# Performance work log

Measured on AMD Instinct MI355X. Metric: run time of the kernel, lower is better.

Reference implementation:

```python
import jax, jax.numpy as jnp
import numpy as np

L = 10           # outer iterations (module arg L -> sinkhorn n_iter)
N_INNER = 1      # n_inner_iter=1 in SinkhornLoss.forward
EPS = 1.0        # entropic regularization epsilon


def setup_inputs() -> dict:
    key = jax.random.key(0)
    kx, ky = jax.random.split(key)
    x = jax.random.normal(kx, (8192, 32), dtype=jnp.float32)
    y = jax.random.normal(ky, (8192, 32), dtype=jnp.float32)
    return {"x": x, "y": y}


def _sinkhorn_loss(x, y):
    n, m = x.shape[0], y.shape[0]
    # sqeuclidean cdist: [n, m]
    C = (x * x).sum(1)[:, None] + (y * y).sum(1)[None, :] - 2.0 * (x @ y.T)
    # uniform marginals mu = 1/n, nu = 1/m (mu=None, nu=None in source)
    logmu = -jnp.log(jnp.asarray(n, C.dtype))
    lognu = -jnp.log(jnp.asarray(m, C.dtype))
    f0 = jnp.zeros((n,), C.dtype)
    g0 = jnp.zeros((m,), C.dtype)

    def body(carry, _):
        f, g = carry
        # log-domain Sinkhorn updates (stable logsumexp form)
        f = EPS * (logmu - jax.nn.logsumexp((g[None, :] - C) / EPS, axis=1))
        g = EPS * (lognu - jax.nn.logsumexp((f[:, None] - C) / EPS, axis=0))
        return (f, g), None

    (f, g), _ = jax.lax.scan(body, (f0, g0), None, length=L * N_INNER)
    gamma = jnp.exp((f[:, None] + g[None, :] - C) / EPS)  # transport plan [n, m]
    return jnp.sum(C * gamma)  # min_cost = <C, gamma>


def reference(x, y):
    return _sinkhorn_loss(x, y)
```

## Files before the change

kernel.cpp:

```cpp
#include <hip/hip_runtime.h>
#include <math.h>


#define KDIM 32
#define NPS 32
#define NSL_LOSS 16
#define LOG2E 1.44269504088896340736f

typedef short short8 __attribute__((ext_vector_type(8)));
typedef float f32x4 __attribute__((ext_vector_type(4)));

__device__ __forceinline__ unsigned short f2bf(float f) {
    unsigned int u = __float_as_uint(f);
    u += 0x7FFF + ((u >> 16) & 1);
    return (unsigned short)(u >> 16);
}
__device__ __forceinline__ float bf2f(unsigned short b) {
    return __uint_as_float(((unsigned int)b) << 16);
}

__global__ void prep_split(const float* __restrict__ x, const float* __restrict__ y,
                           int nelem,
                           unsigned short* __restrict__ xh, unsigned short* __restrict__ xl,
                           unsigned short* __restrict__ yh, unsigned short* __restrict__ yl) {
    int i4 = (blockIdx.x * 256 + threadIdx.x) * 4;
    if (i4 >= 2 * nelem) return;
    const float* src; unsigned short* dh; unsigned short* dl; int off;
    if (i4 < nelem) { src = x; dh = xh; dl = xl; off = i4; }
    else            { src = y; dh = yh; dl = yl; off = i4 - nelem; }
    float4 v = *(const float4*)(src + off);
    ushort4 h, l;
    h.x = f2bf(v.x); l.x = f2bf(v.x - bf2f(h.x));
    h.y = f2bf(v.y); l.y = f2bf(v.y - bf2f(h.y));
    h.z = f2bf(v.z); l.z = f2bf(v.z - bf2f(h.z));
    h.w = f2bf(v.w); l.w = f2bf(v.w - bf2f(h.w));
    *(ushort4*)(dh + off) = h;
    *(ushort4*)(dl + off) = l;
}

__global__ void prep_sq(const float* __restrict__ x, const float* __restrict__ y,
                        int n, float* __restrict__ xsq, float* __restrict__ ysq,
                        float* __restrict__ b_l2e) {
    int i = blockIdx.x * blockDim.x + threadIdx.x;
    if (i >= 2 * n) return;
    const float* src = (i < n) ? x : y;
    int r = (i < n) ? i : i - n;
    const float4* p = (const float4*)(src + (size_t)r * KDIM);
    float s = 0.f;
#pragma unroll
    for (int q = 0; q < 8; ++q) {
        float4 v = p[q];
        s += v.x * v.x + v.y * v.y + v.z * v.z + v.w * v.w;
    }
    if (i < n) xsq[r] = s;
    else { ysq[r] = s; b_l2e[r] = -LOG2E * s; }
}

__global__ __launch_bounds__(256, 4) void sink_pass(
    const unsigned short* __restrict__ Ah, const unsigned short* __restrict__ Alo,
    const unsigned short* __restrict__ Bh, const unsigned short* __restrict__ Blo,
    const float* __restrict__ bias_direct,
    const float* __restrict__ psum_in,
    float* __restrict__ psum_out, int n, float base_l2e) {
    __shared__ float biasl[256];
    __shared__ float red[4][64][17];

    const int tid = threadIdx.x;
    const int w = tid >> 6, lane = tid & 63;
    const int mrow = lane & 15, quad = lane >> 4, koff = quad * 8;
    const int i0 = (blockIdx.x * 4 + w) * 64;
    const int jbeg = blockIdx.y * (n / NPS);

    {
        int c = jbeg + tid;
        float b;
        if (bias_direct) {
            b = bias_direct[c];
        } else {
            float s = 0.f;
#pragma unroll
            for (int k = 0; k < NPS; ++k) s += psum_in[(size_t)k * n + c];
            b = base_l2e - __log2f(s);
        }
        biasl[tid] = b;
    }

    short8 aH[4], aL[4];
#pragma unroll
    for (int t = 0; t < 4; ++t) {
        size_t rb = (size_t)(i0 + t * 16 + mrow) * KDIM + koff;
        aH[t] = *(const short8*)(Ah + rb);
        aL[t] = *(const short8*)(Alo + rb);
    }
    __syncthreads();

    float rs[16];
#pragma unroll
    for (int q = 0; q < 16; ++q) rs[q] = 0.f;
    const float c2 = 2.0f * LOG2E;

    for (int jt = 0; jt < n / NPS; jt += 32) {
        const int j0 = jbeg + jt;
        short8 bH[2], bL[2]; float bc[2];
#pragma unroll
        for (int u = 0; u < 2; ++u) {
            size_t rb = (size_t)(j0 + u * 16 + mrow) * KDIM + koff;
            bH[u] = *(const short8*)(Bh + rb);
            bL[u] = *(const short8*)(Blo + rb);
            bc[u] = biasl[jt + u * 16 + mrow];
        }
#pragma unroll
        for (int t = 0; t < 4; ++t)
#pragma unroll
            for (int u = 0; u < 2; ++u) {
                f32x4 z = {0.f, 0.f, 0.f, 0.f};
                z = __builtin_amdgcn_mfma_f32_16x16x32_bf16(aH[t], bH[u], z, 0, 0, 0);
                z = __builtin_amdgcn_mfma_f32_16x16x32_bf16(aH[t], bL[u], z, 0, 0, 0);
                z = __builtin_amdgcn_mfma_f32_16x16x32_bf16(aL[t], bH[u], z, 0, 0, 0);
#pragma unroll
                for (int r = 0; r < 4; ++r)
                    rs[t * 4 + r] += __builtin_amdgcn_exp2f(fmaf(z[r], c2, bc[u]));
            }
    }

#pragma unroll
    for (int t = 0; t < 4; ++t)
#pragma unroll
        for (int r = 0; r < 4; ++r)
            red[w][t * 16 + quad * 4 + r][mrow] = rs[t * 4 + r];
    __syncthreads();
    {
        int w2 = tid >> 6, row = tid & 63;
        float s = 0.f;
#pragma unroll
        for (int c = 0; c < 16; ++c) s += red[w2][row][c];
        psum_out[(size_t)blockIdx.y * n + (blockIdx.x * 4 + w2) * 64 + row] = s;
    }
}

__global__ __launch_bounds__(256, 4) void sink_loss(
    const unsigned short* __restrict__ Xh, const unsigned short* __restrict__ Xl,
    const unsigned short* __restrict__ Yh, const unsigned short* __restrict__ Yl,
    const float* __restrict__ apsum, const float* __restrict__ bpsum,
    const float* __restrict__ xsq, const float* __restrict__ ysq,
    float* __restrict__ partials, int n, float base_l2e) {
    __shared__ float bcl[512];
    __shared__ float ysl[512];
    __shared__ float arowl[128];
    __shared__ float xsl[128];
    __shared__ float red[256];

    const int tid = threadIdx.x;
    const int w = tid >> 6, lane = tid & 63;
    const int mrow = lane & 15, quad = lane >> 4, koff = quad * 8;
    const int i0 = (blockIdx.x * 4 + w) * 32;
    const int jbeg = blockIdx.y * (n / NSL_LOSS);

#pragma unroll
    for (int h = 0; h < 2; ++h) {
        int c = tid + h * 256;
        int j = jbeg + c;
        float s = 0.f;
#pragma unroll
        for (int k = 0; k < NPS; ++k) s += bpsum[(size_t)k * n + j];
        bcl[c] = base_l2e - __log2f(s);
        ysl[c] = ysq[j];
    }
    if (tid < 128) {
        int i = blockIdx.x * 128 + tid;
        float s = 0.f;
#pragma unroll
        for (int k = 0; k < NPS; ++k) s += apsum[(size_t)k * n + i];
        arowl[tid] = base_l2e - __log2f(s);
        xsl[tid] = xsq[i];
    }

    short8 aH[2], aL[2];
#pragma unroll
    for (int t = 0; t < 2; ++t) {
        size_t rb = (size_t)(i0 + t * 16 + mrow) * KDIM + koff;
        aH[t] = *(const short8*)(Xh + rb);
        aL[t] = *(const short8*)(Xl + rb);
    }
    __syncthreads();

    float ar[8], xs[8];
#pragma unroll
    for (int t = 0; t < 2; ++t)
#pragma unroll
        for (int r = 0; r < 4; ++r) {
            int rl = w * 32 + t * 16 + quad * 4 + r;
            ar[t * 4 + r] = arowl[rl];
            xs[t * 4 + r] = xsl[rl];
        }

    const float c2 = 2.0f * LOG2E;
    float acc = 0.f;

    for (int jt = 0; jt < n / NSL_LOSS; jt += 32) {
        short8 bH[2], bL[2]; float bc[2], ysv[2];
#pragma unroll
        for (int u = 0; u < 2; ++u) {
            int cl = jt + u * 16 + mrow;
            size_t rb = (size_t)(jbeg + cl) * KDIM + koff;
            bH[u] = *(const short8*)(Yh + rb);
            bL[u] = *(const short8*)(Yl + rb);
            bc[u] = bcl[cl];
            ysv[u] = ysl[cl];
        }
#pragma unroll
        for (int t = 0; t < 2; ++t)
#pragma unroll
            for (int u = 0; u < 2; ++u) {
                f32x4 z = {0.f, 0.f, 0.f, 0.f};
                z = __builtin_amdgcn_mfma_f32_16x16x32_bf16(aH[t], bH[u], z, 0, 0, 0);
                z = __builtin_amdgcn_mfma_f32_16x16x32_bf16(aH[t], bL[u], z, 0, 0, 0);
                z = __builtin_amdgcn_mfma_f32_16x16x32_bf16(aL[t], bH[u], z, 0, 0, 0);
#pragma unroll
                for (int r = 0; r < 4; ++r) {
                    float dd = z[r];
                    float wgt = __builtin_amdgcn_exp2f(fmaf(dd, c2, ar[t * 4 + r] + bc[u]));
                    float cst = fmaf(dd, -2.f, xs[t * 4 + r] + ysv[u]);
                    acc = fmaf(cst, wgt, acc);
                }
            }
    }

    red[tid] = acc;
    __syncthreads();
#pragma unroll
    for (int s = 128; s > 0; s >>= 1) {
        if (tid < s) red[tid] += red[tid + s];
        __syncthreads();
    }
    if (tid == 0) partials[blockIdx.y * gridDim.x + blockIdx.x] = red[0];
}

__global__ void sink_reduce(const float* __restrict__ p, int nb,
                            float* __restrict__ out) {
    __shared__ float red[256];
    int tid = threadIdx.x;
    float v = 0.f;
    for (int i = tid; i < nb; i += 256) v += p[i];
    red[tid] = v;
    __syncthreads();
#pragma unroll
    for (int s = 128; s > 0; s >>= 1) {
        if (tid < s) red[tid] += red[tid + s];
        __syncthreads();
    }
    if (tid == 0) out[0] = red[0];
}

extern "C" void kernel_launch(void* const* d_in, const int* in_sizes, int n_in,
                              void* d_out, int out_size, void* d_ws, size_t ws_size,
                              hipStream_t stream) {
    const float* x = (const float*)d_in[0];
    const float* y = (const float*)d_in[1];
    const int n = in_sizes[0] / KDIM;
    const int nelem = n * KDIM;
    const float base_l2e = -LOG2E * logf((float)n);

    float* ws = (float*)d_ws;
    float* xsq   = ws;
    float* ysq   = ws + n;
    float* b_l2e = ws + 2 * n;
    float* apsum = ws + 3 * n;
    float* bpsum = ws + (3 + NPS) * n;
    float* part  = ws + (3 + 2 * NPS) * n;
    unsigned short* us = (unsigned short*)(ws + (4 + 2 * NPS) * n);
    unsigned short* xh = us;
    unsigned short* xl = us + nelem;
    unsigned short* yh = us + 2 * nelem;
    unsigned short* yl = us + 3 * nelem;

    dim3 pgrid(n / 256, NPS);
    dim3 lgrid(n / 128, NSL_LOSS);

    prep_split<<<(2 * nelem / 4 + 255) / 256, 256, 0, stream>>>(x, y, nelem, xh, xl, yh, yl);
    prep_sq<<<(2 * n + 255) / 256, 256, 0, stream>>>(x, y, n, xsq, ysq, b_l2e);

    sink_pass<<<pgrid, 256, 0, stream>>>(xh, xl, yh, yl, b_l2e, nullptr, apsum, n, base_l2e);
    sink_pass<<<pgrid, 256, 0, stream>>>(yh, yl, xh, xl, nullptr, apsum, bpsum, n, base_l2e);
    for (int t = 1; t < 10; ++t) {
        sink_pass<<<pgrid, 256, 0, stream>>>(xh, xl, yh, yl, nullptr, bpsum, apsum, n, base_l2e);
        sink_pass<<<pgrid, 256, 0, stream>>>(yh, yl, xh, xl, nullptr, apsum, bpsum, n, base_l2e);
    }
    sink_loss<<<lgrid, 256, 0, stream>>>(xh, xl, yh, yl, apsum, bpsum, xsq, ysq, part, n, base_l2e);
    sink_reduce<<<1, 256, 0, stream>>>(part, (n / 128) * NSL_LOSS, (float*)d_out);
}
```

Before: 447.9 us.

## Prescale x by 2·log2e, use multiplicative exp-domain potentials, and double-buffer B loads

```diff
diff --git a/kernel.cpp b/kernel.cpp
--- a/kernel.cpp
+++ b/kernel.cpp
@@ -6,6 +6,7 @@
 #define NPS 32
 #define NSL_LOSS 16
 #define LOG2E 1.44269504088896340736f
+#define LN2 0.69314718055994530942f
 
 typedef short short8 __attribute__((ext_vector_type(8)));
 typedef float f32x4 __attribute__((ext_vector_type(4)));
@@ -25,10 +26,11 @@
                            unsigned short* __restrict__ yh, unsigned short* __restrict__ yl) {
     int i4 = (blockIdx.x * 256 + threadIdx.x) * 4;
     if (i4 >= 2 * nelem) return;
-    const float* src; unsigned short* dh; unsigned short* dl; int off;
-    if (i4 < nelem) { src = x; dh = xh; dl = xl; off = i4; }
-    else            { src = y; dh = yh; dl = yl; off = i4 - nelem; }
+    const float* src; unsigned short* dh; unsigned short* dl; int off; float sc;
+    if (i4 < nelem) { src = x; dh = xh; dl = xl; off = i4; sc = 2.0f * LOG2E; }
+    else            { src = y; dh = yh; dl = yl; off = i4 - nelem; sc = 1.0f; }
     float4 v = *(const float4*)(src + off);
+    v.x *= sc; v.y *= sc; v.z *= sc; v.w *= sc;
     ushort4 h, l;
     h.x = f2bf(v.x); l.x = f2bf(v.x - bf2f(h.x));
     h.y = f2bf(v.y); l.y = f2bf(v.y - bf2f(h.y));
@@ -40,7 +42,7 @@
 
 __global__ void prep_sq(const float* __restrict__ x, const float* __restrict__ y,
                         int n, float* __restrict__ xsq, float* __restrict__ ysq,
-                        float* __restrict__ b_l2e) {
+                        float* __restrict__ pb0) {
     int i = blockIdx.x * blockDim.x + threadIdx.x;
     if (i >= 2 * n) return;
     const float* src = (i < n) ? x : y;
@@ -53,16 +55,16 @@
         s += v.x * v.x + v.y * v.y + v.z * v.z + v.w * v.w;
     }
     if (i < n) xsq[r] = s;
-    else { ysq[r] = s; b_l2e[r] = -LOG2E * s; }
+    else { ysq[r] = s; pb0[r] = __builtin_amdgcn_exp2f(-LOG2E * s); }
 }
 
 __global__ __launch_bounds__(256, 4) void sink_pass(
     const unsigned short* __restrict__ Ah, const unsigned short* __restrict__ Alo,
     const unsigned short* __restrict__ Bh, const unsigned short* __restrict__ Blo,
-    const float* __restrict__ bias_direct,
+    const float* __restrict__ pb_direct,
     const float* __restrict__ psum_in,
-    float* __restrict__ psum_out, int n, float base_l2e) {
-    __shared__ float biasl[256];
+    float* __restrict__ psum_out, int n, float inv_n) {
+    __shared__ float pbl[256];
     __shared__ float red[4][64][17];
 
     const int tid = threadIdx.x;
@@ -74,15 +76,15 @@
     {
         int c = jbeg + tid;
         float b;
-        if (bias_direct) {
-            b = bias_direct[c];
+        if (pb_direct) {
+            b = pb_direct[c];
         } else {
             float s = 0.f;
 #pragma unroll
             for (int k = 0; k < NPS; ++k) s += psum_in[(size_t)k * n + c];
-            b = base_l2e - __log2f(s);
+            b = inv_n / s;
         }
-        biasl[tid] = b;
+        pbl[tid] = b;
     }
 
     short8 aH[4], aL[4];
@@ -97,30 +99,41 @@
     float rs[16];
 #pragma unroll
     for (int q = 0; q < 16; ++q) rs[q] = 0.f;
-    const float c2 = 2.0f * LOG2E;
-
-    for (int jt = 0; jt < n / NPS; jt += 32) {
-        const int j0 = jbeg + jt;
-        short8 bH[2], bL[2]; float bc[2];
+
+    auto ldB = [&](int jt, short8* bh, short8* bl, float* pb) {
+        const int j0 = jbeg + jt * 32;
 #pragma unroll
         for (int u = 0; u < 2; ++u) {
             size_t rb = (size_t)(j0 + u * 16 + mrow) * KDIM + koff;
-            bH[u] = *(const short8*)(Bh + rb);
-            bL[u] = *(const short8*)(Blo + rb);
-            bc[u] = biasl[jt + u * 16 + mrow];
+            bh[u] = *(const short8*)(Bh + rb);
+            bl[u] = *(const short8*)(Blo + rb);
+            pb[u] = pbl[jt * 32 + u * 16 + mrow];
         }
+    };
+    auto compute = [&](short8* bh, short8* bl, float* pb) {
 #pragma unroll
         for (int t = 0; t < 4; ++t)
 #pragma unroll
             for (int u = 0; u < 2; ++u) {
                 f32x4 z = {0.f, 0.f, 0.f, 0.f};
-                z = __builtin_amdgcn_mfma_f32_16x16x32_bf16(aH[t], bH[u], z, 0, 0, 0);
-                z = __builtin_amdgcn_mfma_f32_16x16x32_bf16(aH[t], bL[u], z, 0, 0, 0);
-                z = __builtin_amdgcn_mfma_f32_16x16x32_bf16(aL[t], bH[u], z, 0, 0, 0);
+                z = __builtin_amdgcn_mfma_f32_16x16x32_bf16(aH[t], bh[u], z, 0, 0, 0);
+                z = __builtin_amdgcn_mfma_f32_16x16x32_bf16(aH[t], bl[u], z, 0, 0, 0);
+                z = __builtin_amdgcn_mfma_f32_16x16x32_bf16(aL[t], bh[u], z, 0, 0, 0);
 #pragma unroll
                 for (int r = 0; r < 4; ++r)
-                    rs[t * 4 + r] += __builtin_amdgcn_exp2f(fmaf(z[r], c2, bc[u]));
+                    rs[t * 4 + r] = fmaf(__builtin_amdgcn_exp2f(z[r]), pb[u], rs[t * 4 + r]);
             }
+    };
+
+    const int JT = (n / NPS) / 32;
+    short8 bh0[2], bl0[2], bh1[2], bl1[2];
+    float pb0v[2], pb1v[2];
+    ldB(0, bh0, bl0, pb0v);
+    for (int jt = 0; jt < JT; jt += 2) {
+        ldB(jt + 1, bh1, bl1, pb1v);
+        compute(bh0, bl0, pb0v);
+        if (jt + 2 < JT) ldB(jt + 2, bh0, bl0, pb0v);
+        compute(bh1, bl1, pb1v);
     }
 
 #pragma unroll
@@ -143,10 +156,10 @@
     const unsigned short* __restrict__ Yh, const unsigned short* __restrict__ Yl,
     const float* __restrict__ apsum, const float* __restrict__ bpsum,
     const float* __restrict__ xsq, const float* __restrict__ ysq,
-    float* __restrict__ partials, int n, float base_l2e) {
-    __shared__ float bcl[512];
+    float* __restrict__ partials, int n, float inv_n) {
+    __shared__ float pbL[512];
     __shared__ float ysl[512];
-    __shared__ float arowl[128];
+    __shared__ float pal[128];
     __shared__ float xsl[128];
     __shared__ float red[256];
 
@@ -163,7 +176,7 @@
         float s = 0.f;
 #pragma unroll
         for (int k = 0; k < NPS; ++k) s += bpsum[(size_t)k * n + j];
-        bcl[c] = base_l2e - __log2f(s);
+        pbL[c] = inv_n / s;
         ysl[c] = ysq[j];
     }
     if (tid < 128) {
@@ -171,7 +184,7 @@
         float s = 0.f;
 #pragma unroll
         for (int k = 0; k < NPS; ++k) s += apsum[(size_t)k * n + i];
-        arowl[tid] = base_l2e - __log2f(s);
+        pal[tid] = inv_n / s;
         xsl[tid] = xsq[i];
     }
 
@@ -184,46 +197,57 @@
     }
     __syncthreads();
 
-    float ar[8], xs[8];
+    float pa[8], xs[8];
 #pragma unroll
     for (int t = 0; t < 2; ++t)
 #pragma unroll
         for (int r = 0; r < 4; ++r) {
             int rl = w * 32 + t * 16 + quad * 4 + r;
-            ar[t * 4 + r] = arowl[rl];
+            pa[t * 4 + r] = pal[rl];
             xs[t * 4 + r] = xsl[rl];
         }
 
-    const float c2 = 2.0f * LOG2E;
     float acc = 0.f;
 
-    for (int jt = 0; jt < n / NSL_LOSS; jt += 32) {
-        short8 bH[2], bL[2]; float bc[2], ysv[2];
+    auto ldB = [&](int jt, short8* bh, short8* bl, float* pb, float* ysv) {
 #pragma unroll
         for (int u = 0; u < 2; ++u) {
-            int cl = jt + u * 16 + mrow;
+            int cl = jt * 32 + u * 16 + mrow;
             size_t rb = (size_t)(jbeg + cl) * KDIM + koff;
-            bH[u] = *(const short8*)(Yh + rb);
-            bL[u] = *(const short8*)(Yl + rb);
-            bc[u] = bcl[cl];
+            bh[u] = *(const short8*)(Yh + rb);
+            bl[u] = *(const short8*)(Yl + rb);
+            pb[u] = pbL[cl];
             ysv[u] = ysl[cl];
         }
+    };
+    auto compute = [&](short8* bh, short8* bl, float* pb, float* ysv) {
 #pragma unroll
         for (int t = 0; t < 2; ++t)
 #pragma unroll
             for (int u = 0; u < 2; ++u) {
                 f32x4 z = {0.f, 0.f, 0.f, 0.f};
-                z = __builtin_amdgcn_mfma_f32_16x16x32_bf16(aH[t], bH[u], z, 0, 0, 0);
-                z = __builtin_amdgcn_mfma_f32_16x16x32_bf16(aH[t], bL[u], z, 0, 0, 0);
-                z = __builtin_amdgcn_mfma_f32_16x16x32_bf16(aL[t], bH[u], z, 0, 0, 0);
+                z = __builtin_amdgcn_mfma_f32_16x16x32_bf16(aH[t], bh[u], z, 0, 0, 0);
+                z = __builtin_amdgcn_mfma_f32_16x16x32_bf16(aH[t], bl[u], z, 0, 0, 0);
+                z = __builtin_amdgcn_mfma_f32_16x16x32_bf16(aL[t], bh[u], z, 0, 0, 0);
 #pragma unroll
                 for (int r = 0; r < 4; ++r) {
                     float dd = z[r];
-                    float wgt = __builtin_amdgcn_exp2f(fmaf(dd, c2, ar[t * 4 + r] + bc[u]));
-                    float cst = fmaf(dd, -2.f, xs[t * 4 + r] + ysv[u]);
-                    acc = fmaf(cst, wgt, acc);
+                    float e = __builtin_amdgcn_exp2f(dd) * (pa[t * 4 + r] * pb[u]);
+                    float cst = fmaf(dd, -LN2, xs[t * 4 + r] + ysv[u]);
+                    acc = fmaf(cst, e, acc);
                 }
             }
+    };
+
+    const int JT = (n / NSL_LOSS) / 32;
+    short8 bh0[2], bl0[2], bh1[2], bl1[2];
+    float pb0v[2], pb1v[2], ys0v[2], ys1v[2];
+    ldB(0, bh0, bl0, pb0v, ys0v);
+    for (int jt = 0; jt < JT; jt += 2) {
+        ldB(jt + 1, bh1, bl1, pb1v, ys1v);
+        compute(bh0, bl0, pb0v, ys0v);
+        if (jt + 2 < JT) ldB(jt + 2, bh0, bl0, pb0v, ys0v);
+        compute(bh1, bl1, pb1v, ys1v);
     }
 
     red[tid] = acc;
@@ -259,12 +283,12 @@
     const float* y = (const float*)d_in[1];
     const int n = in_sizes[0] / KDIM;
     const int nelem = n * KDIM;
-    const float base_l2e = -LOG2E * logf((float)n);
+    const float inv_n = 1.0f / (float)n;
 
     float* ws = (float*)d_ws;
     float* xsq   = ws;
     float* ysq   = ws + n;
-    float* b_l2e = ws + 2 * n;
+    float* pb0   = ws + 2 * n;
     float* apsum = ws + 3 * n;
     float* bpsum = ws + (3 + NPS) * n;
     float* part  = ws + (3 + 2 * NPS) * n;
@@ -278,14 +302,14 @@
     dim3 lgrid(n / 128, NSL_LOSS);
 
     prep_split<<<(2 * nelem / 4 + 255) / 256, 256, 0, stream>>>(x, y, nelem, xh, xl, yh, yl);
-    prep_sq<<<(2 * n + 255) / 256, 256, 0, stream>>>(x, y, n, xsq, ysq, b_l2e);
-
-    sink_pass<<<pgrid, 256, 0, stream>>>(xh, xl, yh, yl, b_l2e, nullptr, apsum, n, base_l2e);
-    sink_pass<<<pgrid, 256, 0, stream>>>(yh, yl, xh, xl, nullptr, apsum, bpsum, n, base_l2e);
+    prep_sq<<<(2 * n + 255) / 256, 256, 0, stream>>>(x, y, n, xsq, ysq, pb0);
+
+    sink_pass<<<pgrid, 256, 0, stream>>>(xh, xl, yh, yl, pb0, nullptr, apsum, n, inv_n);
+    sink_pass<<<pgrid, 256, 0, stream>>>(yh, yl, xh, xl, nullptr, apsum, bpsum, n, inv_n);
     for (int t = 1; t < 10; ++t) {
-        sink_pass<<<pgrid, 256, 0, stream>>>(xh, xl, yh, yl, nullptr, bpsum, apsum, n, base_l2e);
-        sink_pass<<<pgrid, 256, 0, stream>>>(yh, yl, xh, xl, nullptr, apsum, bpsum, n, base_l2e);
-    }
-    sink_loss<<<lgrid, 256, 0, stream>>>(xh, xl, yh, yl, apsum, bpsum, xsq, ysq, part, n, base_l2e);
+        sink_pass<<<pgrid, 256, 0, stream>>>(xh, xl, yh, yl, nullptr, bpsum, apsum, n, inv_n);
+        sink_pass<<<pgrid, 256, 0, stream>>>(yh, yl, xh, xl, nullptr, apsum, bpsum, n, inv_n);
+    }
+    sink_loss<<<lgrid, 256, 0, stream>>>(xh, xl, yh, yl, apsum, bpsum, xsq, ysq, part, n, inv_n);
     sink_reduce<<<1, 256, 0, stream>>>(part, (n / 128) * NSL_LOSS, (float*)d_out);
 }
```

Measured after the change: 406.0 us. 1.1x faster.
